# Kernel tuning notes

Measured on AMD Instinct MI355X. Metric: run time of the kernel, lower is better.

## Reference

```python
import jax, jax.numpy as jnp
import numpy as np

B, S, D = 2, 1024, 1024
E, K, F, FS = 8, 2, 512, 1024

def setup_inputs() -> dict:
    key = jax.random.key(0)
    ks = jax.random.split(key, 9)
    s = lambda k, shape, fan: jax.random.normal(k, shape, jnp.float32) * (fan ** -0.5)
    return {
        "x": jax.random.normal(ks[0], (B, S, D), jnp.float32),
        "Wr": s(ks[1], (D, E), D),
        "Wg": s(ks[2], (E, D, F), D),
        "Wu": s(ks[3], (E, D, F), D),
        "Wd": s(ks[4], (E, F, D), F),
        "Sg": s(ks[5], (D, FS), D),
        "Su": s(ks[6], (D, FS), D),
        "Sd": s(ks[7], (FS, D), FS),
        "expert_bias": jnp.zeros((E,), jnp.float32),
    }

def reference(x, Wr, Wg, Wu, Wd, Sg, Su, Sd, expert_bias):
    b, s, d = x.shape
    xf = x.reshape(-1, d)                              # [T, D]
    T = xf.shape[0]
    logits = xf @ Wr + expert_bias                     # [T, E]
    top_v, top_i = jax.lax.top_k(logits, K)            # [T, K]
    probs = jax.nn.softmax(top_v, axis=-1)             # [T, K]
    # dense routing-weight matrix: zero for non-selected experts
    rw = jnp.zeros_like(logits).at[jnp.arange(T)[:, None], top_i].set(probs)  # [T, E]
    # SwiGLU experts, computed densely; routing weight zeros out unselected
    gate = jnp.einsum('td,edf->tef', xf, Wg)           # [T, E, F]
    up = jnp.einsum('td,edf->tef', xf, Wu)
    h = jax.nn.silu(gate) * up
    eo = jnp.einsum('tef,efd->ted', h, Wd)             # [T, E, D]
    out = jnp.einsum('te,ted->td', rw, eo)             # [T, D]
    # shared expert applied to all tokens
    out = out + (jax.nn.silu(xf @ Sg) * (xf @ Su)) @ Sd
    return out.reshape(b, s, d)
```

## Files before the change

kernel.cpp:

```cpp
#include <hip/hip_runtime.h>
#include <cstdint>
#include <cstddef>

typedef __attribute__((ext_vector_type(8))) short bf16x8;
typedef __attribute__((ext_vector_type(4))) float f32x4;
typedef __attribute__((ext_vector_type(4))) unsigned short u16x4;

#define AS1 __attribute__((address_space(1)))
#define AS3 __attribute__((address_space(3)))

__device__ __forceinline__ unsigned short f2bf(float f) {
  union { float f; unsigned int u; } v; v.f = f;
  unsigned int r = v.u + 0x7fffu + ((v.u >> 16) & 1u);
  return (unsigned short)(r >> 16);
}

__device__ __forceinline__ void gll16(const unsigned short* g, unsigned short* l) {
  __builtin_amdgcn_global_load_lds((const AS1 void*)g, (AS3 void*)l, 16, 0, 0);
}

__global__ __launch_bounds__(256) void transpose_cvt_all(
    const float* __restrict__ Wg, const float* __restrict__ Wu,
    const float* __restrict__ Wd, const float* __restrict__ Sg,
    const float* __restrict__ Su, const float* __restrict__ Sd,
    const float* __restrict__ x, const float* __restrict__ Wr,
    unsigned short* __restrict__ WguT, unsigned short* __restrict__ WdT,
    unsigned short* __restrict__ SguT, unsigned short* __restrict__ SdT,
    unsigned short* __restrict__ Xb, float* __restrict__ logits) {
  const int z = blockIdx.z;
  const int tid = threadIdx.x;

  if (z == 31) {
    const int bid = blockIdx.y * 16 + blockIdx.x;
    const int wave = tid >> 6;
    const int lane = tid & 63;
#pragma unroll
    for (int it = 0; it < 2; it++) {
      const int t = bid * 8 + wave * 2 + it;
      const float* xr = x + (size_t)t * 1024;
      float acc[8];
#pragma unroll
      for (int e = 0; e < 8; e++) acc[e] = 0.f;
#pragma unroll
      for (int i = 0; i < 16; i++) {
        int d = lane + i * 64;
        float xv = xr[d];
        const float4* w = (const float4*)(Wr + d * 8);
        float4 w0 = w[0], w1 = w[1];
        acc[0] += xv * w0.x; acc[1] += xv * w0.y; acc[2] += xv * w0.z; acc[3] += xv * w0.w;
        acc[4] += xv * w1.x; acc[5] += xv * w1.y; acc[6] += xv * w1.z; acc[7] += xv * w1.w;
      }
#pragma unroll
      for (int off = 32; off > 0; off >>= 1)
#pragma unroll
        for (int e = 0; e < 8; e++) acc[e] += __shfl_down(acc[e], off);
      if (lane == 0) {
#pragma unroll
        for (int e = 0; e < 8; e++) logits[t * 8 + e] = acc[e];
      }
    }
    return;
  }

  if (z >= 27) {
    size_t off = (size_t)(z - 27) * 524288 + blockIdx.y * 32768 + blockIdx.x * 2048 + tid * 8;
    const float4* s = (const float4*)(x + off);
    float4 a = s[0], b = s[1];
    bf16x8 o = { (short)f2bf(a.x), (short)f2bf(a.y), (short)f2bf(a.z), (short)f2bf(a.w),
                 (short)f2bf(b.x), (short)f2bf(b.y), (short)f2bf(b.z), (short)f2bf(b.w) };
    *(bf16x8*)(Xb + off) = o;
    return;
  }

  const float* src; unsigned short* dst; int R, C, drp;
  if (z < 8)       { src = Wg + (size_t)z * 524288; dst = WguT + (size_t)z * 1048576; R = 1024; C = 512; drp = 2048; }
  else if (z < 16) { src = Wu + (size_t)(z - 8) * 524288; dst = WguT + (size_t)(z - 8) * 1048576 + 1024; R = 1024; C = 512; drp = 2048; }
  else if (z < 24) { src = Wd + (size_t)(z - 16) * 524288; dst = WdT + (size_t)(z - 16) * 524288; R = 512; C = 1024; drp = 512; }
  else if (z == 24){ src = Sg; dst = SguT; R = 1024; C = 1024; drp = 2048; }
  else if (z == 25){ src = Su; dst = SguT + 1024; R = 1024; C = 1024; drp = 2048; }
  else             { src = Sd; dst = SdT; R = 1024; C = 1024; drp = 1024; }
  const int c0 = blockIdx.x * 64, r0 = blockIdx.y * 64;
  if (c0 >= C || r0 >= R) return;

  __shared__ float tile[64][65];
  {
    const int row = tid >> 2, cs = (tid & 3) * 16;
    const float* sp = src + (size_t)(r0 + row) * C + c0 + cs;
#pragma unroll
    for (int k = 0; k < 4; k++) {
      float4 v = ((const float4*)sp)[k];
      tile[row][cs + k * 4 + 0] = v.x; tile[row][cs + k * 4 + 1] = v.y;
      tile[row][cs + k * 4 + 2] = v.z; tile[row][cs + k * 4 + 3] = v.w;
    }
  }
  __syncthreads();
#pragma unroll
  for (int i = 0; i < 2; i++) {
    const int cc = i * 32 + (tid >> 3);
    const int rseg = (tid & 7) * 8;
    bf16x8 o;
#pragma unroll
    for (int j = 0; j < 8; j++) o[j] = (short)f2bf(tile[rseg + j][cc]);
    *(bf16x8*)(dst + (size_t)(c0 + cc) * drp + r0 + rseg) = o;
  }
}

__global__ __launch_bounds__(1024) void assign_kernel(
    const float* __restrict__ logits, const float* __restrict__ bias,
    int* __restrict__ list, int* __restrict__ ridx, float* __restrict__ rp,
    int* __restrict__ counts_g, int* __restrict__ offs_g) {
  __shared__ int cnt[8];
  __shared__ int offs[9];
  const int tid = threadIdx.x;
  if (tid < 8) cnt[tid] = 0;
  __syncthreads();
  int te[2][2], tpos[2][2];
  float tp[2][2];
#pragma unroll
  for (int it = 0; it < 2; it++) {
    int t = tid + it * 1024;
    float v[8];
#pragma unroll
    for (int e = 0; e < 8; e++) v[e] = logits[t * 8 + e] + bias[e];
    int i0 = 0;
#pragma unroll
    for (int e = 1; e < 8; e++) if (v[e] > v[i0]) i0 = e;
    int i1 = (i0 == 0) ? 1 : 0;
#pragma unroll
    for (int e = 0; e < 8; e++) if (e != i0 && v[e] > v[i1]) i1 = e;
    float pa = 1.f / (1.f + __expf(v[i1] - v[i0]));
    te[it][0] = i0; te[it][1] = i1;
    tp[it][0] = pa; tp[it][1] = 1.f - pa;
    tpos[it][0] = atomicAdd(&cnt[i0], 1);
    tpos[it][1] = atomicAdd(&cnt[i1], 1);
  }
  __syncthreads();
  if (tid == 0) {
    int s = 0;
#pragma unroll
    for (int e = 0; e < 8; e++) { offs[e] = s; s += cnt[e]; }
    offs[8] = s;
#pragma unroll
    for (int e = 0; e < 8; e++) { counts_g[e] = cnt[e]; offs_g[e] = offs[e]; }
    offs_g[8] = s;
  }
  __syncthreads();
#pragma unroll
  for (int it = 0; it < 2; it++) {
    int t = tid + it * 1024;
#pragma unroll
    for (int k = 0; k < 2; k++) {
      int grow = offs[te[it][k]] + tpos[it][k];
      list[grow] = t;
      ridx[t * 2 + k] = grow;
      rp[t * 2 + k] = tp[it][k];
    }
  }
}

template <int NK>
__device__ __forceinline__ void kloop(
    const unsigned short* ga0, const unsigned short* ga1,
    const unsigned short* gb0, const unsigned short* gb1,
    unsigned short* lwA0, unsigned short* lwA1,
    unsigned short* lwB0, unsigned short* lwB1,
    const unsigned short* lrA, const unsigned short* lrB,
    f32x4 (&acc)[4][4]) {
  gll16(ga0, lwA0);          gll16(ga1, lwA1);
  gll16(gb0, lwB0);          gll16(gb1, lwB1);
  gll16(ga0 + 32, lwA0 + 4096); gll16(ga1 + 32, lwA1 + 4096);
  gll16(gb0 + 32, lwB0 + 4096); gll16(gb1 + 32, lwB1 + 4096);
#pragma unroll
  for (int i = 0; i < NK; ++i) {
    if (i + 1 < NK) asm volatile("s_waitcnt vmcnt(4) lgkmcnt(0)\n\ts_barrier" ::: "memory");
    else            asm volatile("s_waitcnt vmcnt(0) lgkmcnt(0)\n\ts_barrier" ::: "memory");
    if (i + 2 < NK) {
      const int bo = ((i + 2) % 3) * 4096;
      const int ko = (i + 2) * 32;
      gll16(ga0 + ko, lwA0 + bo); gll16(ga1 + ko, lwA1 + bo);
      gll16(gb0 + ko, lwB0 + bo); gll16(gb1 + ko, lwB1 + bo);
    }
    const int ro = (i % 3) * 4096;
    bf16x8 af[4], bf[4];
#pragma unroll
    for (int u = 0; u < 4; ++u) af[u] = *(const bf16x8*)(lrA + ro + u * 512);
#pragma unroll
    for (int u = 0; u < 4; ++u) bf[u] = *(const bf16x8*)(lrB + ro + u * 512);
#pragma unroll
    for (int ii = 0; ii < 4; ++ii)
#pragma unroll
      for (int jj = 0; jj < 4; ++jj)
        acc[ii][jj] = __builtin_amdgcn_mfma_f32_16x16x32_bf16(af[ii], bf[jj], acc[ii][jj], 0, 0, 0);
  }
}

template <int MODE>
__global__ __launch_bounds__(256, 3) void gemm_tn_kernel(
    const unsigned short* __restrict__ Xb, const unsigned short* __restrict__ He,
    const unsigned short* __restrict__ Hs, const unsigned short* __restrict__ Wgu,
    const unsigned short* __restrict__ Sgu, const unsigned short* __restrict__ Wd,
    const unsigned short* __restrict__ Sd, unsigned short* __restrict__ HeOut,
    unsigned short* __restrict__ HsOut, float* __restrict__ De, float* __restrict__ Ds,
    const int* __restrict__ list, const int* __restrict__ counts,
    const int* __restrict__ offs) {
  const int ez = blockIdx.x;
  int cnt, lda, K;
  const unsigned short* A;
  const unsigned short* B;
  const int* alist = nullptr;
  unsigned short* H = nullptr;
  float* D = nullptr;
  int ldh = 0;

  if (MODE == 0) {
    if (ez < 8) {
      if (blockIdx.z >= 8) return;
      cnt = counts[ez]; A = Xb; alist = list + offs[ez]; lda = 1024; K = 1024;
      B = Wgu + (size_t)ez * 1024 * 1024; H = HeOut + (size_t)offs[ez] * 512; ldh = 512;
    } else {
      cnt = 2048; A = Xb; lda = 1024; K = 1024; B = Sgu; H = HsOut; ldh = 1024;
    }
  } else {
    if (ez < 8) {
      cnt = counts[ez]; A = He + (size_t)offs[ez] * 512; lda = 512; K = 512;
      B = Wd + (size_t)ez * 1024 * 512; D = De + (size_t)offs[ez] * 1024;
    } else {
      cnt = 2048; A = Hs; lda = 1024; K = 1024; B = Sd; D = Ds;
    }
  }

  const int m0 = blockIdx.y * 128;
  if (m0 >= cnt) return;
  const int n0 = blockIdx.z * 128;

  __shared__ unsigned short As[3 * 4096];
  __shared__ unsigned short Bs[3 * 4096];

  const int tid = threadIdx.x;
  const int srow = tid >> 2;
  const int scol = (tid & 3) * 8;
  const int wuni = (tid >> 6) * 512;

  int r0 = m0 + srow; if (r0 >= cnt) r0 = cnt - 1;
  int r1 = m0 + srow + 64; if (r1 >= cnt) r1 = cnt - 1;
  size_t abase0, abase1;
  if (MODE == 0 && ez < 8) {
    abase0 = (size_t)alist[r0] * lda; abase1 = (size_t)alist[r1] * lda;
  } else {
    abase0 = (size_t)r0 * lda; abase1 = (size_t)r1 * lda;
  }

  const unsigned short* ga0 = A + abase0 + scol;
  const unsigned short* ga1 = A + abase1 + scol;
  const unsigned short* gb0 = B + (size_t)(n0 + srow) * K + scol;
  const unsigned short* gb1 = B + (size_t)(n0 + srow + 64) * K + scol;

  unsigned short* lwA0 = As + wuni;
  unsigned short* lwA1 = As + 2048 + wuni;
  unsigned short* lwB0 = Bs + wuni;
  unsigned short* lwB1 = Bs + 2048 + wuni;

  const int wave = tid >> 6;
  const int lane = tid & 63;
  const int wm = (wave & 1) * 64;
  const int wn = (wave >> 1) * 64;
  const int fl = lane & 15;
  const int q = lane >> 4;

  const unsigned short* lrA = As + (wm + fl) * 32 + q * 8;
  const unsigned short* lrB = Bs + (wn + fl) * 32 + q * 8;

  f32x4 acc[4][4];
  f32x4 zero = {0.f, 0.f, 0.f, 0.f};
#pragma unroll
  for (int i = 0; i < 4; i++)
#pragma unroll
    for (int j = 0; j < 4; j++) acc[i][j] = zero;

  if (MODE == 1 && ez < 8) kloop<16>(ga0, ga1, gb0, gb1, lwA0, lwA1, lwB0, lwB1, lrA, lrB, acc);
  else                     kloop<32>(ga0, ga1, gb0, gb1, lwA0, lwA1, lwB0, lwB1, lrA, lrB, acc);

  if (MODE == 0) {
#pragma unroll
    for (int i = 0; i < 4; i++) {
#pragma unroll
      for (int j = 0; j < 4; j++) {
#pragma unroll
        for (int r = 0; r < 4; r++) {
          int grow = m0 + wm + i * 16 + q * 4 + r;
          float v = acc[i][j][r];
          float pv = __shfl_xor(v, 1);
          if ((lane & 1) == 0 && grow < cnt) {
            float s = v / (1.f + __expf(-v));
            int colh = (n0 + wn + j * 16 + fl) >> 1;
            H[(size_t)grow * ldh + colh] = f2bf(s * pv);
          }
        }
      }
    }
  } else {
#pragma unroll
    for (int i = 0; i < 4; i++) {
#pragma unroll
      for (int r = 0; r < 4; r++) {
        int grow = m0 + wm + i * 16 + q * 4 + r;
        if (grow >= cnt) continue;
#pragma unroll
        for (int j = 0; j < 4; j++) {
          int col = n0 + wn + j * 16 + fl;
          D[(size_t)grow * 1024 + col] = acc[i][j][r];
        }
      }
    }
  }
}

__global__ __launch_bounds__(256) void combine_kernel(
    const float* __restrict__ Ds, const float* __restrict__ De,
    const int* __restrict__ ridx, const float* __restrict__ rp,
    float* __restrict__ out) {
  const int t = blockIdx.x;
  const int i0 = ridx[t * 2], i1 = ridx[t * 2 + 1];
  const float p0 = rp[t * 2], p1 = rp[t * 2 + 1];
  const float4* a  = (const float4*)(Ds + (size_t)t * 1024);
  const float4* b0 = (const float4*)(De + (size_t)i0 * 1024);
  const float4* b1 = (const float4*)(De + (size_t)i1 * 1024);
  float4* o = (float4*)(out + (size_t)t * 1024);
  int c = threadIdx.x;
  float4 va = a[c], v0 = b0[c], v1 = b1[c];
  float4 r;
  r.x = va.x + p0 * v0.x + p1 * v1.x;
  r.y = va.y + p0 * v0.y + p1 * v1.y;
  r.z = va.z + p0 * v0.z + p1 * v1.z;
  r.w = va.w + p0 * v0.w + p1 * v1.w;
  o[c] = r;
}

extern "C" void kernel_launch(void* const* d_in, const int* in_sizes, int n_in,
                              void* d_out, int out_size, void* d_ws, size_t ws_size,
                              hipStream_t stream) {
  const float* x    = (const float*)d_in[0];
  const float* Wr   = (const float*)d_in[1];
  const float* Wg   = (const float*)d_in[2];
  const float* Wu   = (const float*)d_in[3];
  const float* Wd   = (const float*)d_in[4];
  const float* Sg   = (const float*)d_in[5];
  const float* Su   = (const float*)d_in[6];
  const float* Sd   = (const float*)d_in[7];
  const float* bias = (const float*)d_in[8];
  float* out = (float*)d_out;

  char* ws = (char*)d_ws;
  size_t o = 0;
  auto alloc = [&](size_t b) { char* p = ws + o; o += (b + 255) & ~(size_t)255; return p; };
  unsigned short* Xb   = (unsigned short*)alloc((size_t)2048 * 1024 * 2);
  unsigned short* WguT = (unsigned short*)alloc((size_t)8 * 1024 * 1024 * 2);
  unsigned short* WdT  = (unsigned short*)alloc((size_t)8 * 1024 * 512 * 2);
  unsigned short* SguT = (unsigned short*)alloc((size_t)2048 * 1024 * 2);
  unsigned short* SdT  = (unsigned short*)alloc((size_t)1024 * 1024 * 2);
  float* logits = (float*)alloc((size_t)2048 * 8 * 4);
  int*   list   = (int*)alloc((size_t)4096 * 4);
  int*   ridx   = (int*)alloc((size_t)2048 * 2 * 4);
  float* rp     = (float*)alloc((size_t)2048 * 2 * 4);
  int*   counts = (int*)alloc(64);
  int*   offs   = (int*)alloc(64);
  unsigned short* He = (unsigned short*)alloc((size_t)4096 * 512 * 2);
  unsigned short* Hs = (unsigned short*)alloc((size_t)2048 * 1024 * 2);
  float* De = (float*)alloc((size_t)4096 * 1024 * 4);
  float* Ds = (float*)alloc((size_t)2048 * 1024 * 4);

  transpose_cvt_all<<<dim3(16, 16, 32), 256, 0, stream>>>(Wg, Wu, Wd, Sg, Su, Sd, x, Wr,
                                                          WguT, WdT, SguT, SdT, Xb, logits);

  assign_kernel<<<1, 1024, 0, stream>>>(logits, bias, list, ridx, rp, counts, offs);

  gemm_tn_kernel<0><<<dim3(9, 16, 16), 256, 0, stream>>>(
      Xb, He, Hs, WguT, SguT, WdT, SdT, He, Hs, De, Ds, list, counts, offs);
  gemm_tn_kernel<1><<<dim3(9, 16, 8), 256, 0, stream>>>(
      Xb, He, Hs, WguT, SguT, WdT, SdT, He, Hs, De, Ds, list, counts, offs);

  combine_kernel<<<2048, 256, 0, stream>>>(Ds, De, ridx, rp, out);
}
```

Before: 205.1 us.

## Pre-swizzle weight tiles, use BK=64 double-buffered GEMM with XCD-aware 1D grid

The transpose kernel now writes weights into 128-row panels of 64-wide K slabs with an XOR swizzle, so each GEMM block streams a B tile contiguously. The GEMM moves from BK=32 triple buffering to BK=64 double buffering, with swizzled LDS reads to avoid bank conflicts. The 3D grid becomes a 1D grid mapped so that blocks sharing an expert or shared-expert tiles land on the same XCD (h&7). This targets LDS conflicts, barrier count and L2 locality, at the cost of occupancy dropping from 3 to 2 blocks per CU because LDS use grows.

After: 197.1 us. 3.9% less time.

```diff
diff --git a/kernel.cpp b/kernel.cpp
--- a/kernel.cpp
+++ b/kernel.cpp
@@ -4,7 +4,6 @@
 
 typedef __attribute__((ext_vector_type(8))) short bf16x8;
 typedef __attribute__((ext_vector_type(4))) float f32x4;
-typedef __attribute__((ext_vector_type(4))) unsigned short u16x4;
 
 #define AS1 __attribute__((address_space(1)))
 #define AS3 __attribute__((address_space(3)))
@@ -18,6 +17,7 @@
 __device__ __forceinline__ void gll16(const unsigned short* g, unsigned short* l) {
   __builtin_amdgcn_global_load_lds((const AS1 void*)g, (AS3 void*)l, 16, 0, 0);
 }
+
 
 __global__ __launch_bounds__(256) void transpose_cvt_all(
     const float* __restrict__ Wg, const float* __restrict__ Wu,
@@ -72,13 +72,13 @@
     return;
   }
 
-  const float* src; unsigned short* dst; int R, C, drp;
-  if (z < 8)       { src = Wg + (size_t)z * 524288; dst = WguT + (size_t)z * 1048576; R = 1024; C = 512; drp = 2048; }
-  else if (z < 16) { src = Wu + (size_t)(z - 8) * 524288; dst = WguT + (size_t)(z - 8) * 1048576 + 1024; R = 1024; C = 512; drp = 2048; }
-  else if (z < 24) { src = Wd + (size_t)(z - 16) * 524288; dst = WdT + (size_t)(z - 16) * 524288; R = 512; C = 1024; drp = 512; }
-  else if (z == 24){ src = Sg; dst = SguT; R = 1024; C = 1024; drp = 2048; }
-  else if (z == 25){ src = Su; dst = SguT + 1024; R = 1024; C = 1024; drp = 2048; }
-  else             { src = Sd; dst = SdT; R = 1024; C = 1024; drp = 1024; }
+  const float* src; unsigned short* base; int R, C, nmul, nadd, Ksz;
+  if (z < 8)       { src = Wg + (size_t)z * 524288; base = WguT + (size_t)z * 1048576; R = 1024; C = 512;  nmul = 2; nadd = 0; Ksz = 1024; }
+  else if (z < 16) { src = Wu + (size_t)(z - 8) * 524288; base = WguT + (size_t)(z - 8) * 1048576; R = 1024; C = 512; nmul = 2; nadd = 1; Ksz = 1024; }
+  else if (z < 24) { src = Wd + (size_t)(z - 16) * 524288; base = WdT + (size_t)(z - 16) * 524288; R = 512; C = 1024; nmul = 1; nadd = 0; Ksz = 512; }
+  else if (z == 24){ src = Sg; base = SguT; R = 1024; C = 1024; nmul = 2; nadd = 0; Ksz = 1024; }
+  else if (z == 25){ src = Su; base = SguT; R = 1024; C = 1024; nmul = 2; nadd = 1; Ksz = 1024; }
+  else             { src = Sd; base = SdT; R = 1024; C = 1024; nmul = 1; nadd = 0; Ksz = 1024; }
   const int c0 = blockIdx.x * 64, r0 = blockIdx.y * 64;
   if (c0 >= C || r0 >= R) return;
 
@@ -101,7 +101,11 @@
     bf16x8 o;
 #pragma unroll
     for (int j = 0; j < 8; j++) o[j] = (short)f2bf(tile[rseg + j][cc]);
-    *(bf16x8*)(dst + (size_t)(c0 + cc) * drp + r0 + rseg) = o;
+    const int n = nmul * (c0 + cc) + nadd;
+    const int k0 = r0 + rseg;
+    const int p = n >> 7, r = n & 127, s = k0 >> 6;
+    const int c8 = ((k0 >> 3) & 7) ^ (r & 7);
+    *(bf16x8*)(base + (size_t)p * (Ksz * 128) + (size_t)s * 8192 + (r * 8 + c8) * 8) = o;
   }
 }
 
@@ -158,44 +162,60 @@
   }
 }
 
+#define STAGE8(b, s) \
+  gll16(gA0 + (s) * 64, AsP + (b) * 8192 + wuni); \
+  gll16(gA1 + (s) * 64, AsP + (b) * 8192 + 2048 + wuni); \
+  gll16(gA2 + (s) * 64, AsP + (b) * 8192 + 4096 + wuni); \
+  gll16(gA3 + (s) * 64, AsP + (b) * 8192 + 6144 + wuni); \
+  gll16(gB + (s) * 8192, BsP + (b) * 8192 + wuni); \
+  gll16(gB + (s) * 8192 + 2048, BsP + (b) * 8192 + 2048 + wuni); \
+  gll16(gB + (s) * 8192 + 4096, BsP + (b) * 8192 + 4096 + wuni); \
+  gll16(gB + (s) * 8192 + 6144, BsP + (b) * 8192 + 6144 + wuni);
+
 template <int NK>
-__device__ __forceinline__ void kloop(
-    const unsigned short* ga0, const unsigned short* ga1,
-    const unsigned short* gb0, const unsigned short* gb1,
-    unsigned short* lwA0, unsigned short* lwA1,
-    unsigned short* lwB0, unsigned short* lwB1,
-    const unsigned short* lrA, const unsigned short* lrB,
-    f32x4 (&acc)[4][4]) {
-  gll16(ga0, lwA0);          gll16(ga1, lwA1);
-  gll16(gb0, lwB0);          gll16(gb1, lwB1);
-  gll16(ga0 + 32, lwA0 + 4096); gll16(ga1 + 32, lwA1 + 4096);
-  gll16(gb0 + 32, lwB0 + 4096); gll16(gb1 + 32, lwB1 + 4096);
+__device__ __forceinline__ void kloop64(
+    const unsigned short* gA0, const unsigned short* gA1,
+    const unsigned short* gA2, const unsigned short* gA3,
+    const unsigned short* gB,
+    unsigned short* AsP, unsigned short* BsP, const int wuni,
+    const int aO0, const int aO1, const int aO2, const int aO3,
+    const int bO0, const int bO1, const int bO2, const int bO3,
+    const int cc0, f32x4 (&acc)[4][4]) {
+  STAGE8(0, 0);
 #pragma unroll
   for (int i = 0; i < NK; ++i) {
-    if (i + 1 < NK) asm volatile("s_waitcnt vmcnt(4) lgkmcnt(0)\n\ts_barrier" ::: "memory");
-    else            asm volatile("s_waitcnt vmcnt(0) lgkmcnt(0)\n\ts_barrier" ::: "memory");
-    if (i + 2 < NK) {
-      const int bo = ((i + 2) % 3) * 4096;
-      const int ko = (i + 2) * 32;
-      gll16(ga0 + ko, lwA0 + bo); gll16(ga1 + ko, lwA1 + bo);
-      gll16(gb0 + ko, lwB0 + bo); gll16(gb1 + ko, lwB1 + bo);
-    }
-    const int ro = (i % 3) * 4096;
-    bf16x8 af[4], bf[4];
-#pragma unroll
-    for (int u = 0; u < 4; ++u) af[u] = *(const bf16x8*)(lrA + ro + u * 512);
-#pragma unroll
-    for (int u = 0; u < 4; ++u) bf[u] = *(const bf16x8*)(lrB + ro + u * 512);
-#pragma unroll
-    for (int ii = 0; ii < 4; ++ii)
-#pragma unroll
-      for (int jj = 0; jj < 4; ++jj)
-        acc[ii][jj] = __builtin_amdgcn_mfma_f32_16x16x32_bf16(af[ii], bf[jj], acc[ii][jj], 0, 0, 0);
+    asm volatile("s_waitcnt lgkmcnt(0)\n\ts_barrier" ::: "memory");
+    if (i + 1 < NK) {
+      STAGE8((i + 1) & 1, i + 1);
+      asm volatile("s_waitcnt vmcnt(8)" ::: "memory");
+    } else {
+      asm volatile("s_waitcnt vmcnt(0)" ::: "memory");
+    }
+    const unsigned short* Ab = AsP + (i & 1) * 8192;
+    const unsigned short* Bb = BsP + (i & 1) * 8192;
+#pragma unroll
+    for (int kk = 0; kk < 2; ++kk) {
+      const int co = cc0 ^ (kk << 5);
+      bf16x8 af[4], bf[4];
+      af[0] = *(const bf16x8*)(Ab + aO0 + co);
+      af[1] = *(const bf16x8*)(Ab + aO1 + co);
+      af[2] = *(const bf16x8*)(Ab + aO2 + co);
+      af[3] = *(const bf16x8*)(Ab + aO3 + co);
+      bf[0] = *(const bf16x8*)(Bb + bO0 + co);
+      bf[1] = *(const bf16x8*)(Bb + bO1 + co);
+      bf[2] = *(const bf16x8*)(Bb + bO2 + co);
+      bf[3] = *(const bf16x8*)(Bb + bO3 + co);
+#pragma unroll
+      for (int ii = 0; ii < 4; ++ii)
+#pragma unroll
+        for (int jj = 0; jj < 4; ++jj)
+          acc[ii][jj] = __builtin_amdgcn_mfma_f32_16x16x32_bf16(af[ii], bf[jj], acc[ii][jj], 0, 0, 0);
+    }
   }
 }
 
 template <int MODE>
-__global__ __launch_bounds__(256, 3) void gemm_tn_kernel(
+__global__ __launch_bounds__(256, 2) void gemm_tn_kernel(
     const unsigned short* __restrict__ Xb, const unsigned short* __restrict__ He,
     const unsigned short* __restrict__ Hs, const unsigned short* __restrict__ Wgu,
     const unsigned short* __restrict__ Sgu, const unsigned short* __restrict__ Wd,
@@ -203,62 +223,79 @@
     unsigned short* __restrict__ HsOut, float* __restrict__ De, float* __restrict__ Ds,
     const int* __restrict__ list, const int* __restrict__ counts,
     const int* __restrict__ offs) {
-  const int ez = blockIdx.x;
-  int cnt, lda, K;
+  const int h = blockIdx.x;
+  const int c = h & 7;
+  const int idx = h >> 3;
+
+  int cnt, lda, m0, n0;
+  bool routed;
   const unsigned short* A;
-  const unsigned short* B;
+  const unsigned short* Bt;
   const int* alist = nullptr;
   unsigned short* H = nullptr;
   float* D = nullptr;
   int ldh = 0;
 
   if (MODE == 0) {
-    if (ez < 8) {
-      if (blockIdx.z >= 8) return;
-      cnt = counts[ez]; A = Xb; alist = list + offs[ez]; lda = 1024; K = 1024;
-      B = Wgu + (size_t)ez * 1024 * 1024; H = HeOut + (size_t)offs[ez] * 512; ldh = 512;
+    if (idx < 128) {
+      routed = true;
+      n0 = (idx >> 4) * 128; m0 = (idx & 15) * 128;
+      cnt = counts[c]; A = Xb; alist = list + offs[c]; lda = 1024;
+      Bt = Wgu + (size_t)c * 1048576 + (size_t)(n0 >> 7) * 131072;
+      H = HeOut + (size_t)offs[c] * 512; ldh = 512;
     } else {
-      cnt = 2048; A = Xb; lda = 1024; K = 1024; B = Sgu; H = HsOut; ldh = 1024;
+      routed = false;
+      const int t2 = idx - 128;
+      m0 = ((c & 1) * 8 + (t2 & 7)) * 128;
+      n0 = ((c >> 1) * 4 + (t2 >> 3)) * 128;
+      cnt = 2048; A = Xb; lda = 1024;
+      Bt = Sgu + (size_t)(n0 >> 7) * 131072;
+      H = HsOut; ldh = 1024;
     }
   } else {
-    if (ez < 8) {
-      cnt = counts[ez]; A = He + (size_t)offs[ez] * 512; lda = 512; K = 512;
-      B = Wd + (size_t)ez * 1024 * 512; D = De + (size_t)offs[ez] * 1024;
+    if (idx < 128) {
+      routed = true;
+      n0 = (idx >> 4) * 128; m0 = (idx & 15) * 128;
+      cnt = counts[c]; A = He + (size_t)offs[c] * 512; lda = 512;
+      Bt = Wd + (size_t)c * 524288 + (size_t)(n0 >> 7) * 65536;
+      D = De + (size_t)offs[c] * 1024;
     } else {
-      cnt = 2048; A = Hs; lda = 1024; K = 1024; B = Sd; D = Ds;
-    }
-  }
-
-  const int m0 = blockIdx.y * 128;
+      routed = false;
+      const int t2 = idx - 128;
+      m0 = ((c & 1) * 8 + (t2 & 7)) * 128;
+      n0 = ((c >> 1) * 2 + (t2 >> 3)) * 128;
+      cnt = 2048; A = Hs; lda = 1024;
+      Bt = Sd + (size_t)(n0 >> 7) * 131072;
+      D = Ds;
+    }
+  }
   if (m0 >= cnt) return;
-  const int n0 = blockIdx.z * 128;
-
-  __shared__ unsigned short As[3 * 4096];
-  __shared__ unsigned short Bs[3 * 4096];
+
+  __shared__ unsigned short As[2 * 8192];
+  __shared__ unsigned short Bs[2 * 8192];
 
   const int tid = threadIdx.x;
-  const int srow = tid >> 2;
-  const int scol = (tid & 3) * 8;
   const int wuni = (tid >> 6) * 512;
-
-  int r0 = m0 + srow; if (r0 >= cnt) r0 = cnt - 1;
-  int r1 = m0 + srow + 64; if (r1 >= cnt) r1 = cnt - 1;
-  size_t abase0, abase1;
-  if (MODE == 0 && ez < 8) {
-    abase0 = (size_t)alist[r0] * lda; abase1 = (size_t)alist[r1] * lda;
+  const int qg = ((tid & 7) ^ ((tid >> 3) & 7)) * 8;
+  const int rb = tid >> 3;
+
+  int r0 = m0 + rb;       if (r0 >= cnt) r0 = cnt - 1;
+  int r1 = m0 + 32 + rb;  if (r1 >= cnt) r1 = cnt - 1;
+  int r2 = m0 + 64 + rb;  if (r2 >= cnt) r2 = cnt - 1;
+  int r3 = m0 + 96 + rb;  if (r3 >= cnt) r3 = cnt - 1;
+  size_t ab0, ab1, ab2, ab3;
+  if (MODE == 0 && routed) {
+    ab0 = (size_t)alist[r0] * lda; ab1 = (size_t)alist[r1] * lda;
+    ab2 = (size_t)alist[r2] * lda; ab3 = (size_t)alist[r3] * lda;
   } else {
-    abase0 = (size_t)r0 * lda; abase1 = (size_t)r1 * lda;
-  }
-
-  const unsigned short* ga0 = A + abase0 + scol;
-  const unsigned short* ga1 = A + abase1 + scol;
-  const unsigned short* gb0 = B + (size_t)(n0 + srow) * K + scol;
-  const unsigned short* gb1 = B + (size_t)(n0 + srow + 64) * K + scol;
-
-  unsigned short* lwA0 = As + wuni;
-  unsigned short* lwA1 = As + 2048 + wuni;
-  unsigned short* lwB0 = Bs + wuni;
-  unsigned short* lwB1 = Bs + 2048 + wuni;
+    ab0 = (size_t)r0 * lda; ab1 = (size_t)r1 * lda;
+    ab2 = (size_t)r2 * lda; ab3 = (size_t)r3 * lda;
+  }
+  const unsigned short* gA0 = A + ab0 + qg;
+  const unsigned short* gA1 = A + ab1 + qg;
+  const unsigned short* gA2 = A + ab2 + qg;
+  const unsigned short* gA3 = A + ab3 + qg;
+  const unsigned short* gB = Bt + tid * 8;
 
   const int wave = tid >> 6;
   const int lane = tid & 63;
@@ -267,8 +304,9 @@
   const int fl = lane & 15;
   const int q = lane >> 4;
 
-  const unsigned short* lrA = As + (wm + fl) * 32 + q * 8;
-  const unsigned short* lrB = Bs + (wn + fl) * 32 + q * 8;
+  const int aO0 = (wm + fl) * 64, aO1 = aO0 + 1024, aO2 = aO0 + 2048, aO3 = aO0 + 3072;
+  const int bO0 = (wn + fl) * 64, bO1 = bO0 + 1024, bO2 = bO0 + 2048, bO3 = bO0 + 3072;
+  const int cc0 = (q ^ (fl & 7)) * 8;
 
   f32x4 acc[4][4];
   f32x4 zero = {0.f, 0.f, 0.f, 0.f};
@@ -277,8 +315,10 @@
 #pragma unroll
     for (int j = 0; j < 4; j++) acc[i][j] = zero;
 
-  if (MODE == 1 && ez < 8) kloop<16>(ga0, ga1, gb0, gb1, lwA0, lwA1, lwB0, lwB1, lrA, lrB, acc);
-  else                     kloop<32>(ga0, ga1, gb0, gb1, lwA0, lwA1, lwB0, lwB1, lrA, lrB, acc);
+  if (MODE == 1 && routed)
+    kloop64<8>(gA0, gA1, gA2, gA3, gB, As, Bs, wuni, aO0, aO1, aO2, aO3, bO0, bO1, bO2, bO3, cc0, acc);
+  else
+    kloop64<16>(gA0, gA1, gA2, gA3, gB, As, Bs, wuni, aO0, aO1, aO2, aO3, bO0, bO1, bO2, bO3, cc0, acc);
 
   if (MODE == 0) {
 #pragma unroll
@@ -374,9 +414,9 @@
 
   assign_kernel<<<1, 1024, 0, stream>>>(logits, bias, list, ridx, rp, counts, offs);
 
-  gemm_tn_kernel<0><<<dim3(9, 16, 16), 256, 0, stream>>>(
+  gemm_tn_kernel<0><<<dim3(1280), 256, 0, stream>>>(
       Xb, He, Hs, WguT, SguT, WdT, SdT, He, Hs, De, Ds, list, counts, offs);
-  gemm_tn_kernel<1><<<dim3(9, 16, 8), 256, 0, stream>>>(
+  gemm_tn_kernel<1><<<dim3(1152), 256, 0, stream>>>(
       Xb, He, Hs, WguT, SguT, WdT, SdT, He, Hs, De, Ds, list, counts, offs);
 
   combine_kernel<<<2048, 256, 0, stream>>>(Ds, De, ridx, rp, out);
```
